# Kernel tuning notes

Measured on AMD Instinct MI355X. Metric: run time of the kernel, lower is better.

Reference implementation:

```python
import jax, jax.numpy as jnp
import numpy as np
from jax import lax

B, D_IN, LOW_DIM, NUM_CLASS, MOCO_QUEUE = 4096, 1024, 128, 32, 65536
PROTO_M, MOCO_M, EPS = 0.99, 0.999, 1e-12


def l2norm(x, axis=-1):
    n = jnp.linalg.norm(x, axis=axis, keepdims=True)
    return x / jnp.maximum(n, EPS)


def encoder(x, W_cls, b_cls, W_proj):
    # base_encoder returns (class logits, l2-normalized low-dim embedding)
    return x @ W_cls + b_cls, l2norm(x @ W_proj)


def setup_inputs() -> dict:
    key = jax.random.key(0)
    k = jax.random.split(key, 12)
    img_q = jax.random.normal(k[0], (B, D_IN), jnp.float32)
    im_k = jax.random.normal(k[1], (B, D_IN), jnp.float32)
    true_lab = jax.random.randint(k[2], (B,), 0, NUM_CLASS)
    partial_Y = (jax.random.uniform(k[3], (B, NUM_CLASS)) < 0.3).astype(jnp.float32)
    partial_Y = partial_Y.at[jnp.arange(B), true_lab].set(1.0)  # guarantee nonempty candidate set
    W_cls_q = 0.02 * jax.random.normal(k[4], (D_IN, NUM_CLASS), jnp.float32)
    b_cls_q = jnp.zeros((NUM_CLASS,), jnp.float32)
    W_proj_q = 0.02 * jax.random.normal(k[5], (D_IN, LOW_DIM), jnp.float32)
    # key encoder initialized near query encoder (copied then momentum-drifted)
    W_cls_k = W_cls_q + 0.002 * jax.random.normal(k[6], (D_IN, NUM_CLASS), jnp.float32)
    b_cls_k = jnp.zeros((NUM_CLASS,), jnp.float32)
    W_proj_k = W_proj_q + 0.002 * jax.random.normal(k[7], (D_IN, LOW_DIM), jnp.float32)
    queue = jax.random.normal(k[8], (MOCO_QUEUE, LOW_DIM), jnp.float32)
    queue = queue / jnp.maximum(jnp.linalg.norm(queue, axis=0, keepdims=True), EPS)  # F.normalize(queue, dim=0) as in __init__
    queue_pseudo = jax.random.normal(k[9], (MOCO_QUEUE, NUM_CLASS), jnp.float32)
    queue_partial = jax.random.normal(k[10], (MOCO_QUEUE, NUM_CLASS), jnp.float32)
    prototypes = l2norm(jax.random.normal(k[11], (NUM_CLASS, LOW_DIM), jnp.float32))
    return dict(img_q=img_q, im_k=im_k, partial_Y=partial_Y,
                W_cls_q=W_cls_q, b_cls_q=b_cls_q, W_proj_q=W_proj_q,
                W_cls_k=W_cls_k, b_cls_k=b_cls_k, W_proj_k=W_proj_k,
                prototypes=prototypes, queue=queue,
                queue_pseudo=queue_pseudo, queue_partial=queue_partial)


def reference(img_q, im_k, partial_Y, W_cls_q, b_cls_q, W_proj_q,
              W_cls_k, b_cls_k, W_proj_k, prototypes, queue,
              queue_pseudo, queue_partial):
    output, q = encoder(img_q, W_cls_q, b_cls_q, W_proj_q)
    predicted_scores = jax.nn.softmax(output, axis=1) * partial_Y
    pseudo_labels = jnp.argmax(predicted_scores, axis=1)  # (B,) int
    # prototypes are detached before the similarity (clone().detach())
    score_prot = jax.nn.softmax(q @ lax.stop_gradient(prototypes).T, axis=1)
    # order-dependent per-sample EMA scatter (faithful to the python for-loop,
    # including within-batch label collisions) -> lax.scan recurrence
    qd = lax.stop_gradient(q)
    def step(p, xs):
        feat, lab = xs
        return p.at[lab].set(p[lab] * PROTO_M + (1.0 - PROTO_M) * feat), None
    new_protos, _ = lax.scan(step, lax.stop_gradient(prototypes), (qd, pseudo_labels))
    new_protos = l2norm(new_protos)
    # momentum key-encoder update (no grad), then key features
    Wck = lax.stop_gradient(W_cls_k * MOCO_M + W_cls_q * (1.0 - MOCO_M))
    bck = lax.stop_gradient(b_cls_k * MOCO_M + b_cls_q * (1.0 - MOCO_M))
    Wpk = lax.stop_gradient(W_proj_k * MOCO_M + W_proj_q * (1.0 - MOCO_M))
    _, kfeat = encoder(im_k, Wck, bck, Wpk)
    kfeat = lax.stop_gradient(kfeat)
    qv = lax.stop_gradient(queue)
    qp = lax.stop_gradient(queue_pseudo)
    qpt = lax.stop_gradient(queue_partial)
    features = jnp.concatenate([q, kfeat, qv], axis=0)
    pseudo_scores = jnp.concatenate([predicted_scores, predicted_scores, qp], axis=0)
    partial_target = jnp.concatenate([partial_Y, partial_Y, qpt], axis=0)
    # dequeue-and-enqueue at ptr=0 (buffer state update, no grad)
    new_queue = qv.at[0:B].set(kfeat)
    new_queue_pseudo = qp.at[0:B].set(lax.stop_gradient(predicted_scores))
    new_queue_partial = qpt.at[0:B].set(lax.stop_gradient(partial_Y))
    return (output, features, pseudo_scores, partial_target, score_prot,
            new_protos, new_queue, new_queue_pseudo, new_queue_partial)
```

## Files before the change

### kernel.cpp

```cpp
#include <hip/hip_runtime.h>
#include <hip/hip_bf16.h>
#include <stdint.h>


typedef __attribute__((ext_vector_type(8))) short bf16x8;
typedef __attribute__((ext_vector_type(4))) float f32x4;

constexpr size_t O0 = 0;
constexpr size_t O1 = 131072;
constexpr size_t O2 = 9568256;
constexpr size_t O3 = 11927552;
constexpr size_t O4 = 14286848;
constexpr size_t O5 = 14417920;
constexpr size_t O6 = 14422016;
constexpr size_t O7 = 22810624;
constexpr size_t O8 = 24907776;

__device__ __forceinline__ unsigned short f2b(float x) {
  union { float f; uint32_t u; } v; v.f = x;
  uint32_t u = v.u;
  uint32_t r = (u + 0x7fffu + ((u >> 16) & 1u)) >> 16;
  return (unsigned short)r;
}

__global__ __launch_bounds__(256) void prep(
    const float* __restrict__ Wpq, const float* __restrict__ Wcq,
    const float* __restrict__ Wpk,
    unsigned short* __restrict__ wt_q, unsigned short* __restrict__ wt_pk) {
  const int bid = blockIdx.x;
  const int t = threadIdx.x;
  const float *W1, *W2 = nullptr;
  float a1 = 1.f, a2 = 0.f;
  unsigned short* dst;
  int kb, nbr, nbw, N;
  if (bid < 128) {
    W1 = Wpq; N = 128; kb = (bid & 31) * 32; nbr = nbw = (bid >> 5) * 32;
    dst = wt_q;
  } else if (bid < 160) {
    W1 = Wcq; N = 32; kb = (bid - 128) * 32; nbr = 0; nbw = 128; dst = wt_q;
  } else {
    W1 = Wpk; W2 = Wpq; a1 = 0.999f; a2 = 0.001f; N = 128;
    const int b = bid - 160; kb = (b & 31) * 32; nbr = nbw = (b >> 5) * 32;
    dst = wt_pk;
  }
  __shared__ float tile[32][33];
  const int tx = t & 31, ty = t >> 5;
#pragma unroll
  for (int j = 0; j < 4; ++j) {
    const int k = kb + ty + 8 * j;
    float v = W1[(size_t)k * N + nbr + tx] * a1;
    if (W2) v += W2[(size_t)k * N + nbr + tx] * a2;
    tile[ty + 8 * j][tx] = v;
  }
  __syncthreads();
#pragma unroll
  for (int j = 0; j < 4; ++j) {
    const int n = nbw + ty + 8 * j;
    dst[(size_t)n * 1024 + kb + tx] = f2b(tile[tx][ty + 8 * j]);
  }
}

__global__ __launch_bounds__(320) void mega(
    const float* __restrict__ img_q, const float* __restrict__ im_k,
    const unsigned short* __restrict__ wt_q,
    const unsigned short* __restrict__ wt_pk,
    const float* __restrict__ bias, const float* __restrict__ partialY,
    const float* __restrict__ protos, const float* __restrict__ queue,
    const float* __restrict__ qp, const float* __restrict__ qpt,
    float* __restrict__ out, int* __restrict__ labels) {
  __shared__ __align__(16) unsigned char smem[32768];
  const int bid = blockIdx.x;
  const int t = threadIdx.x;

  if (bid >= 512) {
    constexpr long NQ4 = (long)65536 * 128 / 4;
    constexpr long NP4 = (long)65536 * 32 / 4;
    constexpr long TOT = NQ4 + 2 * NP4;
    float4* o4 = (float4*)out;
    for (long idx = (long)(bid - 512) * 320 + t; idx < TOT; idx += 3072L * 320) {
      if (idx < NQ4) {
        const float4 v = ((const float4*)queue)[idx];
        o4[O1 / 4 + (2L * 4096 * 128) / 4 + idx] = v;
        if ((idx >> 5) >= 4096) o4[O6 / 4 + idx] = v;
      } else if (idx < NQ4 + NP4) {
        const long i = idx - NQ4;
        const float4 v = ((const float4*)qp)[i];
        o4[O2 / 4 + (2L * 4096 * 32) / 4 + i] = v;
        if ((i >> 3) >= 4096) o4[O7 / 4 + i] = v;
      } else {
        const long i = idx - NQ4 - NP4;
        const float4 v = ((const float4*)qpt)[i];
        o4[O3 / 4 + (2L * 4096 * 32) / 4 + i] = v;
        if ((i >> 3) >= 4096) o4[O8 / 4 + i] = v;
      }
    }
    return;
  }

  const int w = t >> 6, l = t & 63;
  const int ar = l & 15, kg = l >> 4;
  const bool isq = bid < 256;
  const int m0 = (isq ? bid : bid - 256) * 16;
  const float* A = isq ? img_q : im_k;
  const unsigned short* Wt = isq ? wt_q : wt_pk;
  const int nstrips = isq ? 5 : 4;

  if (t < 256) {
    const int r = t >> 4, cb = (t & 15) * 4;
    const float* ap = A + (size_t)(m0 + r) * 1024;
    const int sw = (r & 7) << 4;
#pragma unroll
    for (int j = 0; j < 16; ++j) {
      const int col = cb + j * 64;
      const float4 v = *(const float4*)(ap + col);
      uint2 pk;
      pk.x = (uint32_t)f2b(v.x) | ((uint32_t)f2b(v.y) << 16);
      pk.y = (uint32_t)f2b(v.z) | ((uint32_t)f2b(v.w) << 16);
      *(uint2*)(smem + r * 2048 + ((col * 2) ^ sw)) = pk;
    }
  }
  __syncthreads();

  f32x4 acc0 = {0.f, 0.f, 0.f, 0.f}, acc1 = {0.f, 0.f, 0.f, 0.f};
  if (w < nstrips) {
    const int cs = w * 32;
    const unsigned short* b0p = Wt + (size_t)(cs + ar) * 1024;
    const unsigned short* b1p = Wt + (size_t)(cs + 16 + ar) * 1024;
    const int abase = ar * 2048;
    const int asw = (ar & 7) << 4;
#pragma unroll 8
    for (int kk = 0; kk < 32; ++kk) {
      const int k0 = kk * 32 + kg * 8;
      bf16x8 a = *(const bf16x8*)(smem + abase + ((k0 * 2) ^ asw));
      bf16x8 b0 = *(const bf16x8*)(b0p + k0);
      bf16x8 b1 = *(const bf16x8*)(b1p + k0);
      acc0 = __builtin_amdgcn_mfma_f32_16x16x32_bf16(a, b0, acc0, 0, 0, 0);
      acc1 = __builtin_amdgcn_mfma_f32_16x16x32_bf16(a, b1, acc1, 0, 0, 0);
    }
  }
  __syncthreads();

  float* pr = (float*)smem;
  float* Crow = (float*)(smem + 16512);
  if (w < nstrips) {
#pragma unroll
    for (int j = 0; j < 4; ++j) {
      Crow[(kg * 4 + j) * 164 + w * 32 + ar] = acc0[j];
      Crow[(kg * 4 + j) * 164 + w * 32 + 16 + ar] = acc1[j];
    }
  }
  if (isq) {
    for (int i = t; i < 4096; i += 320)
      pr[(i >> 7) * 129 + (i & 127)] = protos[i];
  }
  __syncthreads();

  if (isq) {
    for (int r = w; r < 16; r += 5) {
      const int grow = m0 + r;
      const float* cr = Crow + r * 164;
      float logit = -1e30f;
      if (l < 32) logit = cr[128 + l] + bias[l];
      float m = logit;
      for (int o = 32; o; o >>= 1) m = fmaxf(m, __shfl_xor(m, o));
      const float e = (l < 32) ? __expf(logit - m) : 0.f;
      float ssum = e;
      for (int o = 32; o; o >>= 1) ssum += __shfl_xor(ssum, o);
      const float py = (l < 32) ? partialY[(size_t)grow * 32 + l] : 0.f;
      const float p = e / ssum * py;
      if (l < 32) {
        out[O0 + (size_t)grow * 32 + l] = logit;
        out[O2 + (size_t)grow * 32 + l] = p;
        out[O2 + (size_t)(4096 + grow) * 32 + l] = p;
        out[O7 + (size_t)grow * 32 + l] = p;
        out[O3 + (size_t)grow * 32 + l] = py;
        out[O3 + (size_t)(4096 + grow) * 32 + l] = py;
        out[O8 + (size_t)grow * 32 + l] = py;
      }
      float av = (l < 32) ? p : -1.f;
      int ai = (l < 32) ? l : 1000;
      for (int o = 32; o; o >>= 1) {
        const float ov = __shfl_xor(av, o);
        const int oi = __shfl_xor(ai, o);
        if (ov > av || (ov == av && oi < ai)) { av = ov; ai = oi; }
      }
      if (l == 0) labels[grow] = ai;
      float v0 = cr[l], v1 = cr[64 + l];
      float ss = v0 * v0 + v1 * v1;
      for (int o = 32; o; o >>= 1) ss += __shfl_xor(ss, o);
      const float den = fmaxf(sqrtf(ss), 1e-12f);
      v0 /= den; v1 /= den;
      out[O1 + (size_t)grow * 128 + l] = v0;
      out[O1 + (size_t)grow * 128 + 64 + l] = v1;
      Crow[r * 164 + l] = v0;
      Crow[r * 164 + 64 + l] = v1;
      const int c = l & 31;
      const int dh = (l >> 5) * 64;
      float acc = 0.f;
#pragma unroll
      for (int d = 0; d < 64; ++d)
        acc += Crow[r * 164 + dh + d] * pr[c * 129 + dh + d];
      acc += __shfl_xor(acc, 32);
      float sm = acc;
      for (int o = 16; o; o >>= 1) sm = fmaxf(sm, __shfl_xor(sm, o));
      const float ee = __expf(acc - sm);
      float s2 = ee;
      for (int o = 16; o; o >>= 1) s2 += __shfl_xor(s2, o);
      if (l < 32) out[O4 + (size_t)grow * 32 + l] = ee / s2;
    }
  } else if (w < 4) {
    for (int r = w; r < 16; r += 4) {
      const int grow = m0 + r;
      const float* cr = Crow + r * 164;
      float v0 = cr[l], v1 = cr[64 + l];
      float ss = v0 * v0 + v1 * v1;
      for (int o = 32; o; o >>= 1) ss += __shfl_xor(ss, o);
      const float den = fmaxf(sqrtf(ss), 1e-12f);
      v0 /= den; v1 /= den;
      out[O1 + (size_t)(4096 + grow) * 128 + l] = v0;
      out[O1 + (size_t)(4096 + grow) * 128 + 64 + l] = v1;
      out[O6 + (size_t)grow * 128 + l] = v0;
      out[O6 + (size_t)grow * 128 + 64 + l] = v1;
    }
  }
}

__global__ __launch_bounds__(256) void proto_up(
    const int* __restrict__ labels, const float* __restrict__ protos,
    float* __restrict__ out) {
  __shared__ int lab[4096];
  __shared__ int list[4096];
  __shared__ int wtot[4];
  __shared__ float red[2];
  const int c = blockIdx.x;
  const int t = threadIdx.x;
  const int w = t >> 6, l = t & 63;
  for (int i = t; i < 4096; i += 256) lab[i] = labels[i];
  __syncthreads();
  int cn = 0;
#pragma unroll
  for (int j = 0; j < 16; ++j) {
    const int jj = (j + t) & 15;
    cn += (lab[t * 16 + jj] == c) ? 1 : 0;
  }
  int inc = cn;
  for (int o = 1; o < 64; o <<= 1) {
    const int n = __shfl_up(inc, o);
    if (l >= o) inc += n;
  }
  if (l == 63) wtot[w] = inc;
  __syncthreads();
  int base = 0;
  for (int ww = 0; ww < w; ++ww) base += wtot[ww];
  const int k = wtot[0] + wtot[1] + wtot[2] + wtot[3];
  int off = base + inc - cn;
  for (int j = 0; j < 16; ++j) {
    const int i = t * 16 + j;
    if (lab[i] == c) list[off++] = i;
  }
  __syncthreads();
  float* wf = (float*)lab;
  for (int j = t; j < k; j += 256)
    wf[j] = 0.01f * __powf(0.99f, (float)(k - 1 - j));
  __syncthreads();
  float acc = 0.f;
  if (t < 128) {
    const float* qfeat = out + O1;
    float a0 = protos[(size_t)c * 128 + t] * __powf(0.99f, (float)k);
    float a1 = 0.f, a2 = 0.f, a3 = 0.f;
    int j = 0;
    for (; j + 4 <= k; j += 4) {
      a0 += wf[j]     * qfeat[(size_t)list[j] * 128 + t];
      a1 += wf[j + 1] * qfeat[(size_t)list[j + 1] * 128 + t];
      a2 += wf[j + 2] * qfeat[(size_t)list[j + 2] * 128 + t];
      a3 += wf[j + 3] * qfeat[(size_t)list[j + 3] * 128 + t];
    }
    for (; j < k; ++j) a0 += wf[j] * qfeat[(size_t)list[j] * 128 + t];
    acc = (a0 + a1) + (a2 + a3);
    float ss = acc * acc;
    for (int o = 32; o; o >>= 1) ss += __shfl_xor(ss, o);
    if ((t & 63) == 0) red[t >> 6] = ss;
  }
  __syncthreads();
  if (t < 128)
    out[O5 + (size_t)c * 128 + t] = acc / fmaxf(sqrtf(red[0] + red[1]), 1e-12f);
}

extern "C" void kernel_launch(void* const* d_in, const int* in_sizes, int n_in,
                              void* d_out, int out_size, void* d_ws, size_t ws_size,
                              hipStream_t stream) {
  const float* img_q    = (const float*)d_in[0];
  const float* im_k     = (const float*)d_in[1];
  const float* partialY = (const float*)d_in[2];
  const float* W_cls_q  = (const float*)d_in[3];
  const float* b_cls_q  = (const float*)d_in[4];
  const float* W_proj_q = (const float*)d_in[5];
  const float* W_proj_k = (const float*)d_in[8];
  const float* protos   = (const float*)d_in[9];
  const float* queue    = (const float*)d_in[10];
  const float* queue_ps = (const float*)d_in[11];
  const float* queue_pt = (const float*)d_in[12];
  float* out = (float*)d_out;

  unsigned short* wt_q  = (unsigned short*)d_ws;
  unsigned short* wt_pk = wt_q + 160 * 1024;
  int* labels = (int*)(wt_pk + 128 * 1024);

  prep<<<288, 256, 0, stream>>>(W_proj_q, W_cls_q, W_proj_k, wt_q, wt_pk);
  mega<<<3584, 320, 0, stream>>>(img_q, im_k, wt_q, wt_pk, b_cls_q, partialY,
                                 protos, queue, queue_ps, queue_pt, out,
                                 labels);
  proto_up<<<32, 256, 0, stream>>>(labels, protos, out);
}
```

Before: 239.6 us.

## Pre-swizzle bf16 weights into MFMA fragment order and coalesce A-tile loads

Measured after the change: 232.7 us. -2.9%, faster.

```diff
diff --git a/kernel.cpp b/kernel.cpp
--- a/kernel.cpp
+++ b/kernel.cpp
@@ -32,17 +32,18 @@
   const float *W1, *W2 = nullptr;
   float a1 = 1.f, a2 = 0.f;
   unsigned short* dst;
-  int kb, nbr, nbw, N;
+  int kb, nbr, s, N;
   if (bid < 128) {
-    W1 = Wpq; N = 128; kb = (bid & 31) * 32; nbr = nbw = (bid >> 5) * 32;
-    dst = wt_q;
+    W1 = Wpq; N = 128; kb = (bid & 31) * 32; nbr = (bid >> 5) * 32;
+    s = bid >> 5; dst = wt_q;
   } else if (bid < 160) {
-    W1 = Wcq; N = 32; kb = (bid - 128) * 32; nbr = 0; nbw = 128; dst = wt_q;
+    W1 = Wcq; N = 32; kb = (bid - 128) * 32; nbr = 0; s = 4; dst = wt_q;
   } else {
     W1 = Wpk; W2 = Wpq; a1 = 0.999f; a2 = 0.001f; N = 128;
-    const int b = bid - 160; kb = (b & 31) * 32; nbr = nbw = (b >> 5) * 32;
-    dst = wt_pk;
-  }
+    const int b = bid - 160; kb = (b & 31) * 32; nbr = (b >> 5) * 32;
+    s = b >> 5; dst = wt_pk;
+  }
+  const int kk = (bid < 128) ? (bid & 31) : (bid < 160 ? bid - 128 : ((bid - 160) & 31));
   __shared__ float tile[32][33];
   const int tx = t & 31, ty = t >> 5;
 #pragma unroll
@@ -53,11 +54,15 @@
     tile[ty + 8 * j][tx] = v;
   }
   __syncthreads();
-#pragma unroll
-  for (int j = 0; j < 4; ++j) {
-    const int n = nbw + ty + 8 * j;
-    dst[(size_t)n * 1024 + kb + tx] = f2b(tile[tx][ty + 8 * j]);
-  }
+  const int lf = (t >> 1) & 63;
+  const int half = t >> 7;
+  const int e0 = (t & 1) * 4;
+  const int nloc = half * 16 + (lf & 15);
+  const int kloc = ((lf >> 4) << 3) + e0;
+  uint2 pk;
+  pk.x = (uint32_t)f2b(tile[kloc][nloc]) | ((uint32_t)f2b(tile[kloc + 1][nloc]) << 16);
+  pk.y = (uint32_t)f2b(tile[kloc + 2][nloc]) | ((uint32_t)f2b(tile[kloc + 3][nloc]) << 16);
+  *(uint2*)(dst + (size_t)(s * 32 + kk) * 1024 + t * 4) = pk;
 }
 
 __global__ __launch_bounds__(320) void mega(
@@ -106,34 +111,31 @@
   const int nstrips = isq ? 5 : 4;
 
   if (t < 256) {
-    const int r = t >> 4, cb = (t & 15) * 4;
-    const float* ap = A + (size_t)(m0 + r) * 1024;
-    const int sw = (r & 7) << 4;
+    const int w4 = t >> 6, l6 = t & 63;
 #pragma unroll
     for (int j = 0; j < 16; ++j) {
-      const int col = cb + j * 64;
-      const float4 v = *(const float4*)(ap + col);
+      const int r = w4 * 4 + (j >> 2);
+      const int col = (j & 3) * 256 + l6 * 4;
+      const float4 v = *(const float4*)(A + (size_t)(m0 + r) * 1024 + col);
       uint2 pk;
       pk.x = (uint32_t)f2b(v.x) | ((uint32_t)f2b(v.y) << 16);
       pk.y = (uint32_t)f2b(v.z) | ((uint32_t)f2b(v.w) << 16);
-      *(uint2*)(smem + r * 2048 + ((col * 2) ^ sw)) = pk;
+      *(uint2*)(smem + r * 2048 + ((col * 2) ^ ((r & 7) << 4))) = pk;
     }
   }
   __syncthreads();
 
   f32x4 acc0 = {0.f, 0.f, 0.f, 0.f}, acc1 = {0.f, 0.f, 0.f, 0.f};
   if (w < nstrips) {
-    const int cs = w * 32;
-    const unsigned short* b0p = Wt + (size_t)(cs + ar) * 1024;
-    const unsigned short* b1p = Wt + (size_t)(cs + 16 + ar) * 1024;
+    const unsigned short* bp = Wt + (size_t)(w * 32) * 1024 + l * 8;
     const int abase = ar * 2048;
     const int asw = (ar & 7) << 4;
 #pragma unroll 8
     for (int kk = 0; kk < 32; ++kk) {
       const int k0 = kk * 32 + kg * 8;
       bf16x8 a = *(const bf16x8*)(smem + abase + ((k0 * 2) ^ asw));
-      bf16x8 b0 = *(const bf16x8*)(b0p + k0);
-      bf16x8 b1 = *(const bf16x8*)(b1p + k0);
+      bf16x8 b0 = *(const bf16x8*)(bp + (size_t)kk * 1024);
+      bf16x8 b1 = *(const bf16x8*)(bp + (size_t)kk * 1024 + 512);
       acc0 = __builtin_amdgcn_mfma_f32_16x16x32_bf16(a, b0, acc0, 0, 0, 0);
       acc1 = __builtin_amdgcn_mfma_f32_16x16x32_bf16(a, b1, acc1, 0, 0, 0);
     }
@@ -303,8 +305,8 @@
   float* out = (float*)d_out;
 
   unsigned short* wt_q  = (unsigned short*)d_ws;
-  unsigned short* wt_pk = wt_q + 160 * 1024;
-  int* labels = (int*)(wt_pk + 128 * 1024);
+  unsigned short* wt_pk = wt_q + 5 * 32 * 1024;
+  int* labels = (int*)(wt_pk + 4 * 32 * 1024);
 
   prep<<<288, 256, 0, stream>>>(W_proj_q, W_cls_q, W_proj_k, wt_q, wt_pk);
   mega<<<3584, 320, 0, stream>>>(img_q, im_k, wt_q, wt_pk, b_cls_q, partialY,
```
